# Kernel tuning notes

Hardware: AMD Instinct MI355X
Metric: run time of the kernel (lower is better)

The kernel has to match this reference:

```python
import jax, jax.numpy as jnp
import numpy as np

D = 128

def _intra(nei, h, h_ref, att):
    # att: [2D] split into ref part and neighbor part; leakyrelu(cat(h_ref, nei_emb) @ att)
    a_ref, a_nei = att[:D], att[D:]
    nei_emb = h[nei]                                   # [N, S, D] gather
    s = h_ref @ a_ref                                  # [N]
    s = s[:, None] + nei_emb @ a_nei                   # [N, S]
    w = jax.nn.softmax(jax.nn.leaky_relu(s), axis=1)   # [N, S]
    return jnp.einsum('ns,nsd->nd', w, nei_emb)        # [N, D]

def _inter(embeds, fcW, fcb, att_inter):
    sps = jnp.stack([jnp.tanh(e @ fcW.T + fcb).mean(axis=0) for e in embeds])  # [T, D]
    beta = jax.nn.softmax(sps @ att_inter)             # [T]
    return sum(b * e for b, e in zip(beta, embeds))

def setup_inputs() -> dict:
    key = jax.random.key(0)
    ks = jax.random.split(key, 10)
    N, M, S1, S2 = 50000, 50000, 20, 10
    return {
        'h_ref': jax.random.normal(ks[0], (N, D), jnp.float32),
        'h1': jax.random.normal(ks[1], (M, D), jnp.float32),
        'h2': jax.random.normal(ks[2], (M, D), jnp.float32),
        'nei1': jax.random.randint(ks[3], (N, S1), 0, M),
        'nei2': jax.random.randint(ks[4], (N, S2), 0, M),
        'att1': jax.random.normal(ks[5], (2 * D,), jnp.float32) * 0.1,
        'att2': jax.random.normal(ks[6], (2 * D,), jnp.float32) * 0.1,
        'fcW': jax.random.normal(ks[7], (D, D), jnp.float32) * 0.1,
        'fcb': jnp.zeros((D,), jnp.float32),
        'att_inter': jax.random.normal(ks[8], (D,), jnp.float32) * 0.1,
    }

def reference(h_ref, h1, h2, nei1, nei2, att1, att2, fcW, fcb, att_inter):
    e1 = jax.nn.elu(_intra(nei1, h1, h_ref, att1))
    e2 = jax.nn.elu(_intra(nei2, h2, h_ref, att2))
    return _inter([e1, e2], fcW, fcb, att_inter)
```

## Files before the change

### kernel.cpp

```cpp
#include <hip/hip_runtime.h>
#include <hip/hip_bf16.h>
#include <math.h>

#define D 128
#define NB2 392
#define NWAVES (NB2 * 4)

typedef __attribute__((ext_vector_type(8))) short bf16x8;
typedef __attribute__((ext_vector_type(4))) float f32x4;

__device__ __forceinline__ float wave_sum(float v) {
#pragma unroll
  for (int off = 32; off; off >>= 1) v += __shfl_xor(v, off, 64);
  return v;
}

__device__ __forceinline__ unsigned bfr(float f) {
  const unsigned u = __float_as_uint(f);
  return (u + 0x7FFFu + ((u >> 16) & 1u)) >> 16;
}

__device__ __forceinline__ float fast_tanh(float x) {
  const float ez = __expf(2.f * x);
  return 1.f - 2.f / (ez + 1.f);
}

__global__ __launch_bounds__(256) void k_proj(
    const float* __restrict__ h_ref, const float* __restrict__ h1,
    const float* __restrict__ h2,
    const float* __restrict__ att1, const float* __restrict__ att2,
    const float* __restrict__ fcW, unsigned short* __restrict__ wb,
    float* __restrict__ q1, float* __restrict__ q2,
    float* __restrict__ p1, float* __restrict__ p2,
    unsigned* __restrict__ hb1u, unsigned* __restrict__ hb2u, int N, int M)
{
  const int lane = threadIdx.x & 63;
  const int r = blockIdx.x * 4 + (threadIdx.x >> 6);
  const int total = N + 2 * M + 64;
  if (r >= total) return;
  if (r < N) {
    const float2 v  = *(const float2*)(h_ref + (size_t)r * D + 2 * lane);
    const float2 a1 = *(const float2*)(att1 + 2 * lane);
    const float2 a2 = *(const float2*)(att2 + 2 * lane);
    const float s1 = wave_sum(v.x * a1.x + v.y * a1.y);
    const float s2 = wave_sum(v.x * a2.x + v.y * a2.y);
    if (lane == 0) { q1[r] = s1; q2[r] = s2; }
  } else if (r < N + M) {
    const int m = r - N;
    const float2 v = *(const float2*)(h1 + (size_t)m * D + 2 * lane);
    const float2 a = *(const float2*)(att1 + D + 2 * lane);
    hb1u[(size_t)m * (D / 2) + lane] = (bfr(v.y) << 16) | bfr(v.x);
    const float s = wave_sum(v.x * a.x + v.y * a.y);
    if (lane == 0) p1[m] = s;
  } else if (r < N + 2 * M) {
    const int m = r - N - M;
    const float2 v = *(const float2*)(h2 + (size_t)m * D + 2 * lane);
    const float2 a = *(const float2*)(att2 + D + 2 * lane);
    hb2u[(size_t)m * (D / 2) + lane] = (bfr(v.y) << 16) | bfr(v.x);
    const float s = wave_sum(v.x * a.x + v.y * a.y);
    if (lane == 0) p2[m] = s;
  } else {
    const int base = (r - (N + 2 * M)) * 256 + lane * 4;
    const float4 v = *(const float4*)(fcW + base);
    ushort4 o;
    o.x = (unsigned short)bfr(v.x); o.y = (unsigned short)bfr(v.y);
    o.z = (unsigned short)bfr(v.z); o.w = (unsigned short)bfr(v.w);
    *(ushort4*)(wb + base) = o;
  }
}

template<int S>
__device__ __forceinline__ void intra_body(
    const float* __restrict__ q, const float* __restrict__ p,
    const unsigned* __restrict__ hbu, const int* __restrict__ nei,
    unsigned* __restrict__ eb, int N, int n, int lane)
{
  const int myidx = (lane < S) ? nei[(size_t)n * S + lane] : 0;
  const float pv = (lane < S) ? p[myidx] : 0.f;
  float x = q[n] + pv;
  x = x > 0.f ? x : 0.01f * x;
  if (lane >= S) x = -1e30f;
  float m = x;
#pragma unroll
  for (int off = 32; off; off >>= 1) m = fmaxf(m, __shfl_xor(m, off, 64));
  const float ex = (lane < S) ? __expf(x - m) : 0.f;
  float sum = ex;
#pragma unroll
  for (int off = 32; off; off >>= 1) sum += __shfl_xor(sum, off, 64);
  const float w = ex / sum;

  unsigned uu[S];
#pragma unroll
  for (int s = 0; s < S; ++s) {
    const int row = __shfl(myidx, s, 64);
    uu[s] = hbu[(size_t)row * (D / 2) + lane];
  }
  float ax0 = 0.f, ay0 = 0.f, ax1 = 0.f, ay1 = 0.f;
#pragma unroll
  for (int s = 0; s < S; s += 2) {
    const float w0 = __shfl(w, s, 64);
    const float w1 = __shfl(w, s + 1, 64);
    ax0 = fmaf(w0, __uint_as_float(uu[s] << 16), ax0);
    ay0 = fmaf(w0, __uint_as_float(uu[s] & 0xFFFF0000u), ay0);
    ax1 = fmaf(w1, __uint_as_float(uu[s + 1] << 16), ax1);
    ay1 = fmaf(w1, __uint_as_float(uu[s + 1] & 0xFFFF0000u), ay1);
  }
  float ex2 = ax0 + ax1, ey2 = ay0 + ay1;
  ex2 = ex2 > 0.f ? ex2 : expm1f(ex2);
  ey2 = ey2 > 0.f ? ey2 : expm1f(ey2);
  eb[(size_t)n * (D / 2) + lane] = (bfr(ey2) << 16) | bfr(ex2);
}

template<int SA, int SB>
__global__ __launch_bounds__(256) void k_intra_dual(
    const float* __restrict__ q1, const float* __restrict__ p1,
    const unsigned* __restrict__ hb1, const int* __restrict__ nei1,
    unsigned* __restrict__ eb1,
    const float* __restrict__ q2, const float* __restrict__ p2,
    const unsigned* __restrict__ hb2, const int* __restrict__ nei2,
    unsigned* __restrict__ eb2, int N)
{
  const int lane = threadIdx.x & 63;
  const int n = blockIdx.x * 4 + (threadIdx.x >> 6);
  if (n >= N) return;
  if (blockIdx.y == 0) intra_body<SA>(q1, p1, hb1, nei1, eb1, N, n, lane);
  else                 intra_body<SB>(q2, p2, hb2, nei2, eb2, N, n, lane);
}

__global__ __launch_bounds__(256) void k_intra3_gen(
    const float* __restrict__ q, const float* __restrict__ p,
    const unsigned* __restrict__ hbu, const int* __restrict__ nei,
    unsigned* __restrict__ eb, int N, int S)
{
  const int lane = threadIdx.x & 63;
  const int n = blockIdx.x * 4 + (threadIdx.x >> 6);
  if (n >= N) return;
  const int myidx = (lane < S) ? nei[(size_t)n * S + lane] : 0;
  const float pv = (lane < S) ? p[myidx] : 0.f;
  float x = q[n] + pv;
  x = x > 0.f ? x : 0.01f * x;
  if (lane >= S) x = -1e30f;
  float m = x;
#pragma unroll
  for (int off = 32; off; off >>= 1) m = fmaxf(m, __shfl_xor(m, off, 64));
  const float ex = (lane < S) ? __expf(x - m) : 0.f;
  float sum = ex;
#pragma unroll
  for (int off = 32; off; off >>= 1) sum += __shfl_xor(sum, off, 64);
  const float w = ex / sum;
  float ax = 0.f, ay = 0.f;
  for (int s = 0; s < S; ++s) {
    const int row = __shfl(myidx, s, 64);
    const float ws = __shfl(w, s, 64);
    const unsigned u = hbu[(size_t)row * (D / 2) + lane];
    ax = fmaf(ws, __uint_as_float(u << 16), ax);
    ay = fmaf(ws, __uint_as_float(u & 0xFFFF0000u), ay);
  }
  ax = ax > 0.f ? ax : expm1f(ax);
  ay = ay > 0.f ? ay : expm1f(ay);
  eb[(size_t)n * (D / 2) + lane] = (bfr(ay) << 16) | bfr(ax);
}

__global__ __launch_bounds__(256) void k_fc5(
    const unsigned short* __restrict__ eb1, const unsigned short* __restrict__ eb2,
    const unsigned short* __restrict__ wb, const float* __restrict__ fcb,
    float* __restrict__ part, int N)
{
  const int path = blockIdx.y;
  const unsigned short* __restrict__ eb = path ? eb2 : eb1;
  const int lane = threadIdx.x & 63;
  const int wid  = threadIdx.x >> 6;
  const int wave = blockIdx.x * 4 + wid;
  const int r  = lane & 15;
  const int hi = lane >> 4;

  bf16x8 B[8][4];
#pragma unroll
  for (int jt = 0; jt < 8; ++jt)
#pragma unroll
    for (int kc = 0; kc < 4; ++kc)
      B[jt][kc] = *(const bf16x8*)(wb + (size_t)(jt * 16 + r) * D + kc * 32 + hi * 8);

  float bias[8];
#pragma unroll
  for (int jt = 0; jt < 8; ++jt) bias[jt] = fcb[jt * 16 + r];

  float wsum[8];
#pragma unroll
  for (int jt = 0; jt < 8; ++jt) wsum[jt] = 0.f;

  const int nstrips = (N + 15) / 16;
  for (int st = wave; st < nstrips; st += NWAVES) {
    const int n0 = st * 16;
    int na = n0 + r;
    if (na >= N) na = N - 1;
    const unsigned short* arow = eb + (size_t)na * D + hi * 8;
    bf16x8 A[4];
#pragma unroll
    for (int kc = 0; kc < 4; ++kc) A[kc] = *(const bf16x8*)(arow + kc * 32);

    f32x4 acc[8];
#pragma unroll
    for (int jt = 0; jt < 8; ++jt) acc[jt] = (f32x4){0.f, 0.f, 0.f, 0.f};
#pragma unroll
    for (int kc = 0; kc < 4; ++kc)
#pragma unroll
      for (int jt = 0; jt < 8; ++jt)
        acc[jt] = __builtin_amdgcn_mfma_f32_16x16x32_bf16(A[kc], B[jt][kc], acc[jt], 0, 0, 0);

#pragma unroll
    for (int jt = 0; jt < 8; ++jt) {
      float s = 0.f;
#pragma unroll
      for (int q = 0; q < 4; ++q) {
        const int node = n0 + hi * 4 + q;
        const float t = fast_tanh(acc[jt][q] + bias[jt]);
        s += (node < N) ? t : 0.f;
      }
      s += __shfl_xor(s, 16, 64);
      s += __shfl_xor(s, 32, 64);
      wsum[jt] += s;
    }
  }

  __shared__ float sd[4][D];
  if (lane < 16) {
#pragma unroll
    for (int jt = 0; jt < 8; ++jt) sd[wid][jt * 16 + lane] = wsum[jt];
  }
  __syncthreads();
  const int t = threadIdx.x;
  if (t < D) {
    const float v = sd[0][t] + sd[1][t] + sd[2][t] + sd[3][t];
    part[((size_t)path * NB2 + blockIdx.x) * D + t] = v;
  }
}

__global__ __launch_bounds__(1024) void k_finish(
    const float* __restrict__ part, const float* __restrict__ att_inter,
    float* __restrict__ beta, float invN)
{
  const int t     = threadIdx.x;
  const int j     = t & 127;
  const int path  = (t >> 7) & 1;
  const int chunk = t >> 8;
  const int rows  = NB2 / 4;

  const float* __restrict__ p =
      part + (size_t)path * NB2 * D + (size_t)chunk * rows * D + j;
  float s = 0.f;
#pragma unroll 7
  for (int b = 0; b < rows; ++b) s += p[(size_t)b * D];

  __shared__ float sd[4][2][D];
  sd[chunk][path][j] = s;
  __syncthreads();

  if (t < 256) {
    const float tot = sd[0][path][j] + sd[1][path][j] + sd[2][path][j] + sd[3][path][j];
    float v = (tot * invN) * att_inter[j];
    v = wave_sum(v);
    __shared__ float red[4];
    const int wid = t >> 6;
    if ((t & 63) == 0) red[wid] = v;
    __syncthreads();
    if (t == 0) {
      const float v0 = red[0] + red[1];
      const float v1 = red[2] + red[3];
      const float m = fmaxf(v0, v1);
      const float p0 = __expf(v0 - m), p1 = __expf(v1 - m);
      const float inv = 1.f / (p0 + p1);
      beta[0] = p0 * inv;
      beta[1] = p1 * inv;
    }
  }
}

__global__ __launch_bounds__(256) void k_combine(
    const uint2* __restrict__ eb1v, const uint2* __restrict__ eb2v,
    const float* __restrict__ beta, float* __restrict__ outp, int total4)
{
  const float b0 = beta[0], b1 = beta[1];
  float4* out = (float4*)outp;
  int i = blockIdx.x * 256 + threadIdx.x;
  const int stride = gridDim.x * 256;
  for (; i < total4; i += stride) {
    const uint2 a = eb1v[i], b = eb2v[i];
    float4 o;
    o.x = b0 * __uint_as_float(a.x << 16)         + b1 * __uint_as_float(b.x << 16);
    o.y = b0 * __uint_as_float(a.x & 0xFFFF0000u) + b1 * __uint_as_float(b.x & 0xFFFF0000u);
    o.z = b0 * __uint_as_float(a.y << 16)         + b1 * __uint_as_float(b.y << 16);
    o.w = b0 * __uint_as_float(a.y & 0xFFFF0000u) + b1 * __uint_as_float(b.y & 0xFFFF0000u);
    out[i] = o;
  }
}

extern "C" void kernel_launch(void* const* d_in, const int* in_sizes, int n_in,
                              void* d_out, int out_size, void* d_ws, size_t ws_size,
                              hipStream_t stream) {
  const float* h_ref     = (const float*)d_in[0];
  const float* h1        = (const float*)d_in[1];
  const float* h2        = (const float*)d_in[2];
  const int*   nei1      = (const int*)d_in[3];
  const int*   nei2      = (const int*)d_in[4];
  const float* att1      = (const float*)d_in[5];
  const float* att2      = (const float*)d_in[6];
  const float* fcW       = (const float*)d_in[7];
  const float* fcb       = (const float*)d_in[8];
  const float* att_inter = (const float*)d_in[9];

  const int N  = in_sizes[0] / D;
  const int M  = in_sizes[1] / D;
  const int S1 = in_sizes[3] / N;
  const int S2 = in_sizes[4] / N;

  unsigned short* hb1 = (unsigned short*)d_ws;
  unsigned short* hb2 = hb1 + (size_t)M * D;
  unsigned short* eb1 = hb2 + (size_t)M * D;
  unsigned short* eb2 = eb1 + (size_t)N * D;
  unsigned short* wb  = eb2 + (size_t)N * D;
  float* part = (float*)(wb + D * D);
  float* beta = part + (size_t)2 * NB2 * D;
  float* q1   = beta + 2;
  float* q2   = q1 + N;
  float* p1   = q2 + N;
  float* p2   = p1 + M;
  float* out  = (float*)d_out;

  unsigned* hb1u = (unsigned*)hb1;
  unsigned* hb2u = (unsigned*)hb2;
  unsigned* eb1u = (unsigned*)eb1;
  unsigned* eb2u = (unsigned*)eb2;

  const int rows = N + 2 * M + 64;
  k_proj<<<(rows + 3) / 4, 256, 0, stream>>>(h_ref, h1, h2, att1, att2, fcW, wb,
                                             q1, q2, p1, p2, hb1u, hb2u, N, M);

  const dim3 gA((N + 3) / 4, 2);
  if (S1 == 20 && S2 == 10)
    k_intra_dual<20, 10><<<gA, 256, 0, stream>>>(q1, p1, hb1u, nei1, eb1u,
                                                 q2, p2, hb2u, nei2, eb2u, N);
  else if (S1 == 10 && S2 == 20)
    k_intra_dual<10, 20><<<gA, 256, 0, stream>>>(q1, p1, hb1u, nei1, eb1u,
                                                 q2, p2, hb2u, nei2, eb2u, N);
  else if (S1 == 10 && S2 == 10)
    k_intra_dual<10, 10><<<gA, 256, 0, stream>>>(q1, p1, hb1u, nei1, eb1u,
                                                 q2, p2, hb2u, nei2, eb2u, N);
  else if (S1 == 20 && S2 == 20)
    k_intra_dual<20, 20><<<gA, 256, 0, stream>>>(q1, p1, hb1u, nei1, eb1u,
                                                 q2, p2, hb2u, nei2, eb2u, N);
  else {
    const dim3 g1((N + 3) / 4);
    k_intra3_gen<<<g1, 256, 0, stream>>>(q1, p1, hb1u, nei1, eb1u, N, S1);
    k_intra3_gen<<<g1, 256, 0, stream>>>(q2, p2, hb2u, nei2, eb2u, N, S2);
  }

  const dim3 gB(NB2, 2);
  k_fc5<<<gB, 256, 0, stream>>>(eb1, eb2, wb, fcb, part, N);

  k_finish<<<1, 1024, 0, stream>>>(part, att_inter, beta, 1.0f / (float)N);

  const int total4 = N * D / 4;
  int gD = (total4 + 255) / 256;
  if (gD > 2048) gD = 2048;
  k_combine<<<gD, 256, 0, stream>>>((const uint2*)eb1, (const uint2*)eb2, beta, out, total4);
}
```

Before: 119.3 us.

## Split intra attention into per-thread softmax weights kernel and wave gather kernel

Splits the fused intra-attention kernel in two. The first kernel computes the softmax weights with one thread per node and writes them to a new workspace buffer. The second kernel reads the indices and weights as scalar loads after readfirstlane and does the bf16 row gather without cross-lane shuffles. This removes the per-wave shuffle reductions and the dependent p[] lookup from the gather path, at the cost of an extra launch and a round trip of the weights through global memory.

Measured after the change: 124.1 us. +4.0%, slower.

```diff
diff --git a/kernel.cpp b/kernel.cpp
--- a/kernel.cpp
+++ b/kernel.cpp
@@ -70,61 +70,87 @@
 }
 
 template<int S>
-__device__ __forceinline__ void intra_body(
+__device__ __forceinline__ void weights_body(
     const float* __restrict__ q, const float* __restrict__ p,
-    const unsigned* __restrict__ hbu, const int* __restrict__ nei,
-    unsigned* __restrict__ eb, int N, int n, int lane)
-{
-  const int myidx = (lane < S) ? nei[(size_t)n * S + lane] : 0;
-  const float pv = (lane < S) ? p[myidx] : 0.f;
-  float x = q[n] + pv;
-  x = x > 0.f ? x : 0.01f * x;
-  if (lane >= S) x = -1e30f;
-  float m = x;
-#pragma unroll
-  for (int off = 32; off; off >>= 1) m = fmaxf(m, __shfl_xor(m, off, 64));
-  const float ex = (lane < S) ? __expf(x - m) : 0.f;
-  float sum = ex;
-#pragma unroll
-  for (int off = 32; off; off >>= 1) sum += __shfl_xor(sum, off, 64);
-  const float w = ex / sum;
+    const int* __restrict__ nei, float* __restrict__ wgt, int N, int n)
+{
+  if (n >= N) return;
+  const int* __restrict__ nr = nei + (size_t)n * S;
+  float xs[S];
+  const float qn = q[n];
+  float mx = -1e30f;
+#pragma unroll
+  for (int s = 0; s < S; ++s) {
+    float x = qn + p[nr[s]];
+    x = x > 0.f ? x : 0.01f * x;
+    xs[s] = x;
+    mx = fmaxf(mx, x);
+  }
+  float sum = 0.f;
+#pragma unroll
+  for (int s = 0; s < S; ++s) { xs[s] = __expf(xs[s] - mx); sum += xs[s]; }
+  const float inv = 1.f / sum;
+  float* __restrict__ wr = wgt + (size_t)n * S;
+#pragma unroll
+  for (int s = 0; s < S; ++s) wr[s] = xs[s] * inv;
+}
+
+template<int SA, int SB>
+__global__ __launch_bounds__(256) void k_weights_dual(
+    const float* __restrict__ q1, const float* __restrict__ p1,
+    const int* __restrict__ nei1, float* __restrict__ wgt1,
+    const float* __restrict__ q2, const float* __restrict__ p2,
+    const int* __restrict__ nei2, float* __restrict__ wgt2, int N)
+{
+  const int n = blockIdx.x * 256 + threadIdx.x;
+  if (blockIdx.y == 0) weights_body<SA>(q1, p1, nei1, wgt1, N, n);
+  else                 weights_body<SB>(q2, p2, nei2, wgt2, N, n);
+}
+
+template<int S>
+__device__ __forceinline__ void gather_body(
+    const float* __restrict__ wgt, const unsigned* __restrict__ hbu,
+    const int* __restrict__ nei, unsigned* __restrict__ eb, int N,
+    int n, int lane)
+{
+  n = __builtin_amdgcn_readfirstlane(n);
+  const int* __restrict__ nr = nei + (size_t)n * S;
+  const float* __restrict__ wr = wgt + (size_t)n * S;
+  int rows[S];
+  float ws[S];
+#pragma unroll
+  for (int s = 0; s < S; ++s) rows[s] = nr[s];
+#pragma unroll
+  for (int s = 0; s < S; ++s) ws[s] = wr[s];
 
   unsigned uu[S];
 #pragma unroll
+  for (int s = 0; s < S; ++s)
+    uu[s] = hbu[(size_t)rows[s] * (D / 2) + lane];
+
+  float ax = 0.f, ay = 0.f;
+#pragma unroll
   for (int s = 0; s < S; ++s) {
-    const int row = __shfl(myidx, s, 64);
-    uu[s] = hbu[(size_t)row * (D / 2) + lane];
-  }
-  float ax0 = 0.f, ay0 = 0.f, ax1 = 0.f, ay1 = 0.f;
-#pragma unroll
-  for (int s = 0; s < S; s += 2) {
-    const float w0 = __shfl(w, s, 64);
-    const float w1 = __shfl(w, s + 1, 64);
-    ax0 = fmaf(w0, __uint_as_float(uu[s] << 16), ax0);
-    ay0 = fmaf(w0, __uint_as_float(uu[s] & 0xFFFF0000u), ay0);
-    ax1 = fmaf(w1, __uint_as_float(uu[s + 1] << 16), ax1);
-    ay1 = fmaf(w1, __uint_as_float(uu[s + 1] & 0xFFFF0000u), ay1);
-  }
-  float ex2 = ax0 + ax1, ey2 = ay0 + ay1;
-  ex2 = ex2 > 0.f ? ex2 : expm1f(ex2);
-  ey2 = ey2 > 0.f ? ey2 : expm1f(ey2);
-  eb[(size_t)n * (D / 2) + lane] = (bfr(ey2) << 16) | bfr(ex2);
+    ax = fmaf(ws[s], __uint_as_float(uu[s] << 16), ax);
+    ay = fmaf(ws[s], __uint_as_float(uu[s] & 0xFFFF0000u), ay);
+  }
+  ax = ax > 0.f ? ax : expm1f(ax);
+  ay = ay > 0.f ? ay : expm1f(ay);
+  eb[(size_t)n * (D / 2) + lane] = (bfr(ay) << 16) | bfr(ax);
 }
 
 template<int SA, int SB>
-__global__ __launch_bounds__(256) void k_intra_dual(
-    const float* __restrict__ q1, const float* __restrict__ p1,
-    const unsigned* __restrict__ hb1, const int* __restrict__ nei1,
-    unsigned* __restrict__ eb1,
-    const float* __restrict__ q2, const float* __restrict__ p2,
-    const unsigned* __restrict__ hb2, const int* __restrict__ nei2,
-    unsigned* __restrict__ eb2, int N)
+__global__ __launch_bounds__(256) void k_gather_dual(
+    const float* __restrict__ wgt1, const unsigned* __restrict__ hb1,
+    const int* __restrict__ nei1, unsigned* __restrict__ eb1,
+    const float* __restrict__ wgt2, const unsigned* __restrict__ hb2,
+    const int* __restrict__ nei2, unsigned* __restrict__ eb2, int N)
 {
   const int lane = threadIdx.x & 63;
   const int n = blockIdx.x * 4 + (threadIdx.x >> 6);
   if (n >= N) return;
-  if (blockIdx.y == 0) intra_body<SA>(q1, p1, hb1, nei1, eb1, N, n, lane);
-  else                 intra_body<SB>(q2, p2, hb2, nei2, eb2, N, n, lane);
+  if (blockIdx.y == 0) gather_body<SA>(wgt1, hb1, nei1, eb1, N, n, lane);
+  else                 gather_body<SB>(wgt2, hb2, nei2, eb2, N, n, lane);
 }
 
 __global__ __launch_bounds__(256) void k_intra3_gen(
@@ -151,10 +177,10 @@
   float ax = 0.f, ay = 0.f;
   for (int s = 0; s < S; ++s) {
     const int row = __shfl(myidx, s, 64);
-    const float ws = __shfl(w, s, 64);
+    const float wsv = __shfl(w, s, 64);
     const unsigned u = hbu[(size_t)row * (D / 2) + lane];
-    ax = fmaf(ws, __uint_as_float(u << 16), ax);
-    ay = fmaf(ws, __uint_as_float(u & 0xFFFF0000u), ay);
+    ax = fmaf(wsv, __uint_as_float(u << 16), ax);
+    ay = fmaf(wsv, __uint_as_float(u & 0xFFFF0000u), ay);
   }
   ax = ax > 0.f ? ax : expm1f(ax);
   ay = ay > 0.f ? ay : expm1f(ay);
@@ -325,6 +351,8 @@
   float* q2   = q1 + N;
   float* p1   = q2 + N;
   float* p2   = p1 + M;
+  float* wgt1 = p2 + M;
+  float* wgt2 = wgt1 + (size_t)N * S1;
   float* out  = (float*)d_out;
 
   unsigned* hb1u = (unsigned*)hb1;
@@ -336,20 +364,24 @@
   k_proj<<<(rows + 3) / 4, 256, 0, stream>>>(h_ref, h1, h2, att1, att2, fcW, wb,
                                              q1, q2, p1, p2, hb1u, hb2u, N, M);
 
-  const dim3 gA((N + 3) / 4, 2);
-  if (S1 == 20 && S2 == 10)
-    k_intra_dual<20, 10><<<gA, 256, 0, stream>>>(q1, p1, hb1u, nei1, eb1u,
-                                                 q2, p2, hb2u, nei2, eb2u, N);
-  else if (S1 == 10 && S2 == 20)
-    k_intra_dual<10, 20><<<gA, 256, 0, stream>>>(q1, p1, hb1u, nei1, eb1u,
-                                                 q2, p2, hb2u, nei2, eb2u, N);
-  else if (S1 == 10 && S2 == 10)
-    k_intra_dual<10, 10><<<gA, 256, 0, stream>>>(q1, p1, hb1u, nei1, eb1u,
-                                                 q2, p2, hb2u, nei2, eb2u, N);
-  else if (S1 == 20 && S2 == 20)
-    k_intra_dual<20, 20><<<gA, 256, 0, stream>>>(q1, p1, hb1u, nei1, eb1u,
-                                                 q2, p2, hb2u, nei2, eb2u, N);
-  else {
+  const bool fast = (S1 == 20 || S1 == 10) && (S2 == 20 || S2 == 10);
+  if (fast) {
+    const dim3 gW((N + 255) / 256, 2);
+    const dim3 gG((N + 3) / 4, 2);
+    if (S1 == 20 && S2 == 10) {
+      k_weights_dual<20, 10><<<gW, 256, 0, stream>>>(q1, p1, nei1, wgt1, q2, p2, nei2, wgt2, N);
+      k_gather_dual<20, 10><<<gG, 256, 0, stream>>>(wgt1, hb1u, nei1, eb1u, wgt2, hb2u, nei2, eb2u, N);
+    } else if (S1 == 10 && S2 == 20) {
+      k_weights_dual<10, 20><<<gW, 256, 0, stream>>>(q1, p1, nei1, wgt1, q2, p2, nei2, wgt2, N);
+      k_gather_dual<10, 20><<<gG, 256, 0, stream>>>(wgt1, hb1u, nei1, eb1u, wgt2, hb2u, nei2, eb2u, N);
+    } else if (S1 == 10 && S2 == 10) {
+      k_weights_dual<10, 10><<<gW, 256, 0, stream>>>(q1, p1, nei1, wgt1, q2, p2, nei2, wgt2, N);
+      k_gather_dual<10, 10><<<gG, 256, 0, stream>>>(wgt1, hb1u, nei1, eb1u, wgt2, hb2u, nei2, eb2u, N);
+    } else {
+      k_weights_dual<20, 20><<<gW, 256, 0, stream>>>(q1, p1, nei1, wgt1, q2, p2, nei2, wgt2, N);
+      k_gather_dual<20, 20><<<gG, 256, 0, stream>>>(wgt1, hb1u, nei1, eb1u, wgt2, hb2u, nei2, eb2u, N);
+    }
+  } else {
     const dim3 g1((N + 3) / 4);
     k_intra3_gen<<<g1, 256, 0, stream>>>(q1, p1, hb1u, nei1, eb1u, N, S1);
     k_intra3_gen<<<g1, 256, 0, stream>>>(q2, p2, hb2u, nei2, eb2u, N, S2);
```

## Process two nodes per wave in intra attention with shared-memory softmax weights

Applied to the files above, without the earlier changes.

Restructures the neighbor-attention kernel so each block handles 8 nodes. The softmax scores are computed by 32 threads, 4 lanes per node, and stored in shared memory, and each wave then gathers and accumulates two nodes. The aim is to raise memory-level parallelism with more outstanding gathers per wave and to cut redundant shuffle-based reductions. In exchange it adds a block barrier, register pressure from two sets of S gathered rows, and redundant per-lane neighbor index loads.

Result: slower. 123.2 us (+3.2%).

```diff
diff --git a/kernel.cpp b/kernel.cpp
--- a/kernel.cpp
+++ b/kernel.cpp
@@ -5,6 +5,7 @@
 #define D 128
 #define NB2 392
 #define NWAVES (NB2 * 4)
+#define TILE 8
 
 typedef __attribute__((ext_vector_type(8))) short bf16x8;
 typedef __attribute__((ext_vector_type(4))) float f32x4;
@@ -70,49 +71,98 @@
 }
 
 template<int S>
-__device__ __forceinline__ void intra_body(
+__device__ __forceinline__ void intra4_body(
     const float* __restrict__ q, const float* __restrict__ p,
     const unsigned* __restrict__ hbu, const int* __restrict__ nei,
-    unsigned* __restrict__ eb, int N, int n, int lane)
-{
-  const int myidx = (lane < S) ? nei[(size_t)n * S + lane] : 0;
-  const float pv = (lane < S) ? p[myidx] : 0.f;
-  float x = q[n] + pv;
-  x = x > 0.f ? x : 0.01f * x;
-  if (lane >= S) x = -1e30f;
-  float m = x;
-#pragma unroll
-  for (int off = 32; off; off >>= 1) m = fmaxf(m, __shfl_xor(m, off, 64));
-  const float ex = (lane < S) ? __expf(x - m) : 0.f;
-  float sum = ex;
-#pragma unroll
-  for (int off = 32; off; off >>= 1) sum += __shfl_xor(sum, off, 64);
-  const float w = ex / sum;
-
-  unsigned uu[S];
+    unsigned* __restrict__ eb, int N, float (*lw)[S])
+{
+  const int tid = threadIdx.x;
+  const int nb = blockIdx.x * TILE;
+
+  if (tid < TILE * 4) {
+    const int nl = tid >> 2, qi = tid & 3;
+    const int n = nb + nl;
+    if (n < N) {
+      constexpr int CNT = (S + 3) / 4;
+      const int* __restrict__ nr = nei + (size_t)n * S;
+      const float qn = q[n];
+      float xs[CNT];
+      float mx = -1e30f;
+#pragma unroll
+      for (int k = 0; k < CNT; ++k) {
+        const int s = qi * CNT + k;
+        float x = -1e30f;
+        if (s < S) {
+          const float pv = p[nr[s]];
+          x = qn + pv;
+          x = x > 0.f ? x : 0.01f * x;
+        }
+        xs[k] = x;
+        mx = fmaxf(mx, x);
+      }
+      mx = fmaxf(mx, __shfl_xor(mx, 1, 64));
+      mx = fmaxf(mx, __shfl_xor(mx, 2, 64));
+      float sum = 0.f;
+#pragma unroll
+      for (int k = 0; k < CNT; ++k) { xs[k] = __expf(xs[k] - mx); sum += xs[k]; }
+      sum += __shfl_xor(sum, 1, 64);
+      sum += __shfl_xor(sum, 2, 64);
+      const float inv = 1.f / sum;
+#pragma unroll
+      for (int k = 0; k < CNT; ++k) {
+        const int s = qi * CNT + k;
+        if (s < S) lw[nl][s] = xs[k] * inv;
+      }
+    }
+  }
+  __syncthreads();
+
+  const int lane = tid & 63, wid = tid >> 6;
+  const int na = nb + wid * 2;
+  if (na >= N) return;
+  const int nbn = na + 1;
+  const bool two = (nbn < N);
+
+  const int* __restrict__ nrA = nei + (size_t)na * S;
+  const int* __restrict__ nrB = nei + (size_t)(two ? nbn : na) * S;
+  int rA[S], rB[S];
+#pragma unroll
+  for (int s = 0; s < S; ++s) rA[s] = nrA[s];
+#pragma unroll
+  for (int s = 0; s < S; ++s) rB[s] = nrB[s];
+
+  unsigned uA[S], uB[S];
+#pragma unroll
+  for (int s = 0; s < S; ++s) uA[s] = hbu[(size_t)rA[s] * (D / 2) + lane];
+#pragma unroll
+  for (int s = 0; s < S; ++s) uB[s] = hbu[(size_t)rB[s] * (D / 2) + lane];
+
+  const int nlA = wid * 2, nlB = wid * 2 + 1;
+  float ax = 0.f, ay = 0.f, bx = 0.f, by = 0.f;
 #pragma unroll
   for (int s = 0; s < S; ++s) {
-    const int row = __shfl(myidx, s, 64);
-    uu[s] = hbu[(size_t)row * (D / 2) + lane];
-  }
-  float ax0 = 0.f, ay0 = 0.f, ax1 = 0.f, ay1 = 0.f;
-#pragma unroll
-  for (int s = 0; s < S; s += 2) {
-    const float w0 = __shfl(w, s, 64);
-    const float w1 = __shfl(w, s + 1, 64);
-    ax0 = fmaf(w0, __uint_as_float(uu[s] << 16), ax0);
-    ay0 = fmaf(w0, __uint_as_float(uu[s] & 0xFFFF0000u), ay0);
-    ax1 = fmaf(w1, __uint_as_float(uu[s + 1] << 16), ax1);
-    ay1 = fmaf(w1, __uint_as_float(uu[s + 1] & 0xFFFF0000u), ay1);
-  }
-  float ex2 = ax0 + ax1, ey2 = ay0 + ay1;
-  ex2 = ex2 > 0.f ? ex2 : expm1f(ex2);
-  ey2 = ey2 > 0.f ? ey2 : expm1f(ey2);
-  eb[(size_t)n * (D / 2) + lane] = (bfr(ey2) << 16) | bfr(ex2);
+    const float wA = lw[nlA][s];
+    ax = fmaf(wA, __uint_as_float(uA[s] << 16), ax);
+    ay = fmaf(wA, __uint_as_float(uA[s] & 0xFFFF0000u), ay);
+  }
+#pragma unroll
+  for (int s = 0; s < S; ++s) {
+    const float wB = two ? lw[nlB][s] : 0.f;
+    bx = fmaf(wB, __uint_as_float(uB[s] << 16), bx);
+    by = fmaf(wB, __uint_as_float(uB[s] & 0xFFFF0000u), by);
+  }
+  ax = ax > 0.f ? ax : expm1f(ax);
+  ay = ay > 0.f ? ay : expm1f(ay);
+  eb[(size_t)na * (D / 2) + lane] = (bfr(ay) << 16) | bfr(ax);
+  if (two) {
+    bx = bx > 0.f ? bx : expm1f(bx);
+    by = by > 0.f ? by : expm1f(by);
+    eb[(size_t)nbn * (D / 2) + lane] = (bfr(by) << 16) | bfr(bx);
+  }
 }
 
 template<int SA, int SB>
-__global__ __launch_bounds__(256) void k_intra_dual(
+__global__ __launch_bounds__(256) void k_intra4_dual(
     const float* __restrict__ q1, const float* __restrict__ p1,
     const unsigned* __restrict__ hb1, const int* __restrict__ nei1,
     unsigned* __restrict__ eb1,
@@ -120,11 +170,13 @@
     const unsigned* __restrict__ hb2, const int* __restrict__ nei2,
     unsigned* __restrict__ eb2, int N)
 {
-  const int lane = threadIdx.x & 63;
-  const int n = blockIdx.x * 4 + (threadIdx.x >> 6);
-  if (n >= N) return;
-  if (blockIdx.y == 0) intra_body<SA>(q1, p1, hb1, nei1, eb1, N, n, lane);
-  else                 intra_body<SB>(q2, p2, hb2, nei2, eb2, N, n, lane);
+  if (blockIdx.y == 0) {
+    __shared__ float lwA[TILE][SA];
+    intra4_body<SA>(q1, p1, hb1, nei1, eb1, N, lwA);
+  } else {
+    __shared__ float lwB[TILE][SB];
+    intra4_body<SB>(q2, p2, hb2, nei2, eb2, N, lwB);
+  }
 }
 
 __global__ __launch_bounds__(256) void k_intra3_gen(
@@ -151,10 +203,10 @@
   float ax = 0.f, ay = 0.f;
   for (int s = 0; s < S; ++s) {
     const int row = __shfl(myidx, s, 64);
-    const float ws = __shfl(w, s, 64);
+    const float wsv = __shfl(w, s, 64);
     const unsigned u = hbu[(size_t)row * (D / 2) + lane];
-    ax = fmaf(ws, __uint_as_float(u << 16), ax);
-    ay = fmaf(ws, __uint_as_float(u & 0xFFFF0000u), ay);
+    ax = fmaf(wsv, __uint_as_float(u << 16), ax);
+    ay = fmaf(wsv, __uint_as_float(u & 0xFFFF0000u), ay);
   }
   ax = ax > 0.f ? ax : expm1f(ax);
   ay = ay > 0.f ? ay : expm1f(ay);
@@ -336,20 +388,22 @@
   k_proj<<<(rows + 3) / 4, 256, 0, stream>>>(h_ref, h1, h2, att1, att2, fcW, wb,
                                              q1, q2, p1, p2, hb1u, hb2u, N, M);
 
-  const dim3 gA((N + 3) / 4, 2);
-  if (S1 == 20 && S2 == 10)
-    k_intra_dual<20, 10><<<gA, 256, 0, stream>>>(q1, p1, hb1u, nei1, eb1u,
-                                                 q2, p2, hb2u, nei2, eb2u, N);
-  else if (S1 == 10 && S2 == 20)
-    k_intra_dual<10, 20><<<gA, 256, 0, stream>>>(q1, p1, hb1u, nei1, eb1u,
-                                                 q2, p2, hb2u, nei2, eb2u, N);
-  else if (S1 == 10 && S2 == 10)
-    k_intra_dual<10, 10><<<gA, 256, 0, stream>>>(q1, p1, hb1u, nei1, eb1u,
-                                                 q2, p2, hb2u, nei2, eb2u, N);
-  else if (S1 == 20 && S2 == 20)
-    k_intra_dual<20, 20><<<gA, 256, 0, stream>>>(q1, p1, hb1u, nei1, eb1u,
-                                                 q2, p2, hb2u, nei2, eb2u, N);
-  else {
+  const bool fast = (S1 == 20 || S1 == 10) && (S2 == 20 || S2 == 10);
+  if (fast) {
+    const dim3 gI((N + TILE - 1) / TILE, 2);
+    if (S1 == 20 && S2 == 10)
+      k_intra4_dual<20, 10><<<gI, 256, 0, stream>>>(q1, p1, hb1u, nei1, eb1u,
+                                                    q2, p2, hb2u, nei2, eb2u, N);
+    else if (S1 == 10 && S2 == 20)
+      k_intra4_dual<10, 20><<<gI, 256, 0, stream>>>(q1, p1, hb1u, nei1, eb1u,
+                                                    q2, p2, hb2u, nei2, eb2u, N);
+    else if (S1 == 10 && S2 == 10)
+      k_intra4_dual<10, 10><<<gI, 256, 0, stream>>>(q1, p1, hb1u, nei1, eb1u,
+                                                    q2, p2, hb2u, nei2, eb2u, N);
+    else
+      k_intra4_dual<20, 20><<<gI, 256, 0, stream>>>(q1, p1, hb1u, nei1, eb1u,
+                                                    q2, p2, hb2u, nei2, eb2u, N);
+  } else {
     const dim3 g1((N + 3) / 4);
     k_intra3_gen<<<g1, 256, 0, stream>>>(q1, p1, hb1u, nei1, eb1u, N, S1);
     k_intra3_gen<<<g1, 256, 0, stream>>>(q2, p2, hb2u, nei2, eb2u, N, S2);
```
